# Kernel optimization log

Measured on AMD Instinct MI355X. Metric: run time of the kernel, lower is better.

The kernel has to match this reference:

```python
import jax, jax.numpy as jnp
import numpy as np

N = 30000        # nodes
E = 480000       # edges (before self-loops)
F_IN = 512       # input feature dim
HID = 64         # per-head hidden dim
HEADS = 4
WIDTH = HID * HEADS  # 256, concat heads
LAYERS = 3
NCLS = 40
NEG_SLOPE = 0.2


def setup_inputs() -> dict:
    key = jax.random.key(0)
    ks = jax.random.split(key, 16)
    def p(k, shape, scale=0.1):
        return jax.random.normal(k, shape, dtype=jnp.float32) * scale
    return {
        "x": jax.random.normal(ks[0], (N, F_IN), dtype=jnp.float32),
        "edge_index": jax.random.randint(ks[1], (2, E), 0, N, dtype=jnp.int32),
        # layer 1: F_IN -> HEADS*HID (concat)
        "W1": p(ks[2], (F_IN, WIDTH)), "as1": p(ks[3], (HEADS, HID)), "ad1": p(ks[4], (HEADS, HID)), "b1": p(ks[5], (WIDTH,)),
        # layer 2: WIDTH -> WIDTH
        "W2": p(ks[6], (WIDTH, WIDTH)), "as2": p(ks[7], (HEADS, HID)), "ad2": p(ks[8], (HEADS, HID)), "b2": p(ks[9], (WIDTH,)),
        # layer 3: WIDTH -> WIDTH
        "W3": p(ks[10], (WIDTH, WIDTH)), "as3": p(ks[11], (HEADS, HID)), "ad3": p(ks[12], (HEADS, HID)), "b3": p(ks[13], (WIDTH,)),
        # JK='cat' output head: WIDTH*LAYERS -> NCLS
        "Wo": p(ks[14], (WIDTH * LAYERS, NCLS)), "bo": p(ks[15], (NCLS,)),
    }


def gat_layer(x, Wm, a_src, a_dst, b, src, dst):
    # PyG GATConv (concat=True, eval mode): h = xW reshaped [N,H,C];
    # e_ij = leaky_relu(a_src.h_j + a_dst.h_i) for edge j->i, softmax over dst groups.
    n = x.shape[0]
    H, C = a_src.shape
    h = (x @ Wm).reshape(n, H, C)                      # [N,H,C]
    es = jnp.sum(h * a_src, axis=-1)                   # [N,H]
    ed = jnp.sum(h * a_dst, axis=-1)                   # [N,H]
    e = jax.nn.leaky_relu(es[src] + ed[dst], NEG_SLOPE)  # [Etot,H]
    m = jax.ops.segment_max(e, dst, num_segments=n)    # stable softmax per dst node
    w = jnp.exp(e - m[dst])
    den = jax.ops.segment_sum(w, dst, num_segments=n)
    alpha = w / den[dst]                               # [Etot,H]
    out = jax.ops.segment_sum(h[src] * alpha[:, :, None], dst, num_segments=n)  # [N,H,C]
    return out.reshape(n, H * C) + b


def reference(x, edge_index, W1, as1, ad1, b1, W2, as2, ad2, b2, W3, as3, ad3, b3, Wo, bo):
    # add self-loops (PyG GATConv default)
    loops = jnp.arange(N, dtype=edge_index.dtype)
    src = jnp.concatenate([edge_index[0], loops])
    dst = jnp.concatenate([edge_index[1], loops])
    # dropout is identity in eval mode
    h1 = jax.nn.relu(gat_layer(x, W1, as1, ad1, b1, src, dst))
    h2 = jax.nn.relu(gat_layer(h1, W2, as2, ad2, b2, src, dst))
    h3 = jax.nn.relu(gat_layer(h2, W3, as3, ad3, b3, src, dst))
    h = jnp.concatenate([h1, h2, h3], axis=-1)         # JK 'cat': [N, WIDTH*LAYERS]
    return h @ Wo + bo                                 # [N, NCLS]
```

## Files before the change

### kernel.cpp

```cpp
#include <hip/hip_runtime.h>

#define N_NODES 30000
#define N_EDGES 480000
#define ETOT    510000
#define F_IN    512
#define WIDTH   256
#define NCLS    40
#define KCAT    768
#define NPAD    48

typedef __attribute__((ext_vector_type(8))) short short8;
typedef __attribute__((ext_vector_type(4))) float f32x4;

__device__ __forceinline__ unsigned short f2bf(float f){
  unsigned u = __float_as_uint(f);
  u += 0x7fffu + ((u >> 16) & 1u);
  return (unsigned short)(u >> 16);
}
__device__ __forceinline__ float b2f(unsigned short s){
  return __uint_as_float(((unsigned)s) << 16);
}

__global__ void transpose_w_kernel(const float* __restrict__ W, unsigned short* __restrict__ Wt,
                                   int K, int Nc){
  int k = blockIdx.x * blockDim.x + threadIdx.x;
  int n = blockIdx.y;
  if (k < K) Wt[(size_t)n * K + k] = f2bf(W[(size_t)k * Nc + n]);
}

__global__ void transpose_wo_kernel(const float* __restrict__ Wo, unsigned short* __restrict__ WoT){
  int i = blockIdx.x * blockDim.x + threadIdx.x;
  if (i < NPAD * KCAT){
    int c = i / KCAT, k = i - c * KCAT;
    WoT[i] = (c < NCLS) ? f2bf(Wo[(size_t)k * NCLS + c]) : (unsigned short)0;
  }
}

__global__ void zero_kernel(int* __restrict__ p, int n){
  int i = blockIdx.x * blockDim.x + threadIdx.x;
  if (i < n) p[i] = 0;
}

__global__ void hist_kernel(const int* __restrict__ ei, int* __restrict__ counts){
  int e = blockIdx.x * blockDim.x + threadIdx.x;
  if (e < ETOT){
    int d = (e < N_EDGES) ? ei[N_EDGES + e] : (e - N_EDGES);
    atomicAdd(&counts[d], 1);
  }
}

__global__ __launch_bounds__(1024) void scan_kernel(const int* __restrict__ counts,
                                                    int* __restrict__ offsets,
                                                    int* __restrict__ cursor, int n){
  __shared__ int wsum[16];
  int tid = threadIdx.x, lane = tid & 63, wid = tid >> 6;
  int running = 0;
  int nchunks = (n + 1023) >> 10;
  for (int ch = 0; ch < nchunks; ++ch){
    int i = (ch << 10) + tid;
    int v = (i < n) ? counts[i] : 0;
    int x = v;
    #pragma unroll
    for (int off = 1; off < 64; off <<= 1){
      int t = __shfl_up(x, off, 64);
      if (lane >= off) x += t;
    }
    if (lane == 63) wsum[wid] = x;
    __syncthreads();
    if (wid == 0){
      int s = (lane < 16) ? wsum[lane] : 0;
      #pragma unroll
      for (int off = 1; off < 16; off <<= 1){
        int t = __shfl_up(s, off, 64);
        if (lane >= off) s += t;
      }
      if (lane < 16) wsum[lane] = s;
    }
    __syncthreads();
    int waveprefix = (wid > 0) ? wsum[wid - 1] : 0;
    int excl = x - v + waveprefix + running;
    if (i < n){ offsets[i] = excl; cursor[i] = excl; }
    running += wsum[15];
    __syncthreads();
  }
  if (tid == 0) offsets[n] = running;
}

__global__ void scatter_kernel(const int* __restrict__ ei, int* __restrict__ cursor,
                               int* __restrict__ srcs){
  int e = blockIdx.x * blockDim.x + threadIdx.x;
  if (e < ETOT){
    int s, d;
    if (e < N_EDGES){ s = ei[e]; d = ei[N_EDGES + e]; }
    else { s = e - N_EDGES; d = s; }
    int pos = atomicAdd(&cursor[d], 1);
    srcs[pos] = s;
  }
}

#define BM 64
#define BK 32
#define LDA 40

template<bool AF32>
__global__ __launch_bounds__(256) void gemm_fused_kernel(const void* __restrict__ Araw,
                                                         const unsigned short* __restrict__ Bt,
                                                         const float* __restrict__ a_s,
                                                         const float* __restrict__ a_d,
                                                         float* __restrict__ es,
                                                         float* __restrict__ ed,
                                                         unsigned short* __restrict__ hb,
                                                         int M, int K){
  __shared__ unsigned short Als[BM * LDA];
  __shared__ unsigned short Bls[256 * LDA];
  int tid = threadIdx.x;
  int lane = tid & 63, wid = tid >> 6;
  int l15 = lane & 15, quad = lane >> 4;
  int m0 = blockIdx.x * BM;

  f32x4 acc[16];
  #pragma unroll
  for (int t = 0; t < 16; ++t) acc[t] = (f32x4){0.f, 0.f, 0.f, 0.f};

  for (int k0 = 0; k0 < K; k0 += BK){
    __syncthreads();
    {
      int row = tid >> 2, g = tid & 3;
      int grow = m0 + row; if (grow >= M) grow = M - 1;
      if (AF32){
        const float* Af = (const float*)Araw + (size_t)grow * K + k0 + 8 * g;
        float4 v0 = *(const float4*)(Af);
        float4 v1 = *(const float4*)(Af + 4);
        ushort4 p0 = {f2bf(v0.x), f2bf(v0.y), f2bf(v0.z), f2bf(v0.w)};
        ushort4 p1 = {f2bf(v1.x), f2bf(v1.y), f2bf(v1.z), f2bf(v1.w)};
        *(ushort4*)(&Als[row * LDA + 8 * g])     = p0;
        *(ushort4*)(&Als[row * LDA + 8 * g + 4]) = p1;
      } else {
        const unsigned short* Ab = (const unsigned short*)Araw;
        uint4 av = *(const uint4*)(Ab + (size_t)grow * K + k0 + 8 * g);
        *(uint4*)(&Als[row * LDA + 8 * g]) = av;
      }
      const unsigned short* src = Bt + (size_t)tid * K + k0;
      uint4 b0 = *(const uint4*)(src);
      uint4 b1 = *(const uint4*)(src + 8);
      uint4 b2 = *(const uint4*)(src + 16);
      uint4 b3 = *(const uint4*)(src + 24);
      unsigned short* dst = &Bls[tid * LDA];
      *(uint4*)(dst) = b0;
      *(uint4*)(dst + 8) = b1;
      *(uint4*)(dst + 16) = b2;
      *(uint4*)(dst + 24) = b3;
    }
    __syncthreads();
    short8 af = *(const short8*)(&Als[(16 * wid + l15) * LDA + quad * 8]);
    #pragma unroll
    for (int t = 0; t < 16; ++t){
      short8 bf = *(const short8*)(&Bls[(16 * t + l15) * LDA + quad * 8]);
      acc[t] = __builtin_amdgcn_mfma_f32_16x16x32_bf16(af, bf, acc[t], 0, 0, 0);
    }
  }

  int row0 = m0 + 16 * wid + quad * 4;

  #pragma unroll
  for (int t = 0; t < 16; ++t){
    int col = 16 * t + l15;
    #pragma unroll
    for (int r = 0; r < 4; ++r){
      int grow = row0 + r;
      if (grow < M) hb[(size_t)grow * WIDTH + col] = f2bf(acc[t][r]);
    }
  }

  float as_v[16], ad_v[16];
  #pragma unroll
  for (int t = 0; t < 16; ++t){
    int cc = 16 * (t & 3) + l15;
    as_v[t] = a_s[(t >> 2) * 64 + cc];
    ad_v[t] = a_d[(t >> 2) * 64 + cc];
  }
  #pragma unroll
  for (int h = 0; h < 4; ++h){
    #pragma unroll
    for (int r = 0; r < 4; ++r){
      float se = 0.f, sd = 0.f;
      #pragma unroll
      for (int tt = 0; tt < 4; ++tt){
        int t = 4 * h + tt;
        se += acc[t][r] * as_v[t];
        sd += acc[t][r] * ad_v[t];
      }
      #pragma unroll
      for (int off = 1; off < 16; off <<= 1){
        se += __shfl_xor(se, off, 64);
        sd += __shfl_xor(sd, off, 64);
      }
      int grow = row0 + r;
      if (l15 == 0 && grow < M){
        es[grow * 4 + h] = se;
        ed[grow * 4 + h] = sd;
      }
    }
  }
}

__global__ __launch_bounds__(256) void agg_kernel(const int* __restrict__ offsets,
                                                  const int* __restrict__ srcs,
                                                  const float* __restrict__ es,
                                                  const float* __restrict__ ed,
                                                  const unsigned short* __restrict__ hb,
                                                  const float* __restrict__ bias,
                                                  unsigned short* __restrict__ hout){
  __shared__ float eLds[8][64][4];
  __shared__ int   sLds[8][64];
  int wid = threadIdx.x >> 6;
  int lane = threadIdx.x & 63;
  int half = lane >> 5, l32 = lane & 31;
  int slot = wid * 2 + half;
  int n = blockIdx.x * 8 + slot;
  int base = offsets[n];
  int deg = offsets[n + 1] - base;
  float4 edv = *(const float4*)(ed + n * 4);

  float m0 = -1e30f, m1 = -1e30f, m2 = -1e30f, m3 = -1e30f;
  for (int i = l32; i < deg; i += 32){
    int s = srcs[base + i];
    float4 ev = *(const float4*)(es + s * 4);
    float e0 = ev.x + edv.x, e1 = ev.y + edv.y, e2 = ev.z + edv.z, e3 = ev.w + edv.w;
    e0 = e0 > 0.f ? e0 : 0.2f * e0;
    e1 = e1 > 0.f ? e1 : 0.2f * e1;
    e2 = e2 > 0.f ? e2 : 0.2f * e2;
    e3 = e3 > 0.f ? e3 : 0.2f * e3;
    if (i < 64){
      sLds[slot][i] = s;
      *(float4*)(&eLds[slot][i][0]) = (float4){e0, e1, e2, e3};
    }
    m0 = fmaxf(m0, e0); m1 = fmaxf(m1, e1); m2 = fmaxf(m2, e2); m3 = fmaxf(m3, e3);
  }
  #pragma unroll
  for (int off = 1; off < 32; off <<= 1){
    m0 = fmaxf(m0, __shfl_xor(m0, off, 64));
    m1 = fmaxf(m1, __shfl_xor(m1, off, 64));
    m2 = fmaxf(m2, __shfl_xor(m2, off, 64));
    m3 = fmaxf(m3, __shfl_xor(m3, off, 64));
  }
  int head = l32 >> 3;
  float mh  = (head == 0) ? m0 : (head == 1) ? m1 : (head == 2) ? m2 : m3;
  float edh = (head == 0) ? edv.x : (head == 1) ? edv.y : (head == 2) ? edv.z : edv.w;

  float2 a0 = {0.f,0.f}, a1 = {0.f,0.f}, a2 = {0.f,0.f}, a3 = {0.f,0.f};
  float den = 0.f;
  const unsigned short* hcol = hb + 8 * l32;
  for (int i = 0; i < deg; i += 8){
    int sidx[8]; float w[8];
    #pragma unroll
    for (int u = 0; u < 8; ++u){
      int idx = i + u;
      bool v = idx < deg;
      float le; int s;
      if (idx < 64 || !v){
        int ic = v ? idx : 0;
        if (ic >= 64) ic = 0;
        s  = sLds[slot][ic];
        le = eLds[slot][ic][head];
      } else {
        s = srcs[base + idx];
        float e = es[s * 4 + head] + edh;
        le = e > 0.f ? e : 0.2f * e;
      }
      sidx[u] = s;
      w[u] = v ? __expf(le - mh) : 0.f;
    }
    uint4 hv[8];
    #pragma unroll
    for (int u = 0; u < 8; ++u)
      hv[u] = *(const uint4*)(hcol + (size_t)sidx[u] * WIDTH);
    #pragma unroll
    for (int u = 0; u < 8; ++u){
      float wu = w[u];
      den += wu;
      a0.x += wu * __uint_as_float(hv[u].x << 16);
      a0.y += wu * __uint_as_float(hv[u].x & 0xffff0000u);
      a1.x += wu * __uint_as_float(hv[u].y << 16);
      a1.y += wu * __uint_as_float(hv[u].y & 0xffff0000u);
      a2.x += wu * __uint_as_float(hv[u].z << 16);
      a2.y += wu * __uint_as_float(hv[u].z & 0xffff0000u);
      a3.x += wu * __uint_as_float(hv[u].w << 16);
      a3.y += wu * __uint_as_float(hv[u].w & 0xffff0000u);
    }
  }
  float inv = 1.0f / den;
  const float* bp = bias + 8 * l32;
  float4 bv0 = *(const float4*)(bp);
  float4 bv1 = *(const float4*)(bp + 4);
  float o0 = fmaxf(a0.x * inv + bv0.x, 0.f);
  float o1 = fmaxf(a0.y * inv + bv0.y, 0.f);
  float o2 = fmaxf(a1.x * inv + bv0.z, 0.f);
  float o3 = fmaxf(a1.y * inv + bv0.w, 0.f);
  float o4 = fmaxf(a2.x * inv + bv1.x, 0.f);
  float o5 = fmaxf(a2.y * inv + bv1.y, 0.f);
  float o6 = fmaxf(a3.x * inv + bv1.z, 0.f);
  float o7 = fmaxf(a3.y * inv + bv1.w, 0.f);
  uint4 o;
  o.x = (unsigned)f2bf(o0) | ((unsigned)f2bf(o1) << 16);
  o.y = (unsigned)f2bf(o2) | ((unsigned)f2bf(o3) << 16);
  o.z = (unsigned)f2bf(o4) | ((unsigned)f2bf(o5) << 16);
  o.w = (unsigned)f2bf(o6) | ((unsigned)f2bf(o7) << 16);
  *(uint4*)(hout + (size_t)n * WIDTH + 8 * l32) = o;
}

__global__ __launch_bounds__(256) void out_gemm_kernel(const unsigned short* __restrict__ h1,
                                                       const unsigned short* __restrict__ h2,
                                                       const unsigned short* __restrict__ h3,
                                                       const unsigned short* __restrict__ WoT,
                                                       const float* __restrict__ bo,
                                                       float* __restrict__ out){
  int tid = threadIdx.x, lane = tid & 63, wid = tid >> 6;
  int l15 = lane & 15, quad = lane >> 4;
  int m0 = blockIdx.x * 64 + 16 * wid;

  f32x4 acc[3];
  #pragma unroll
  for (int t = 0; t < 3; ++t) acc[t] = (f32x4){0.f, 0.f, 0.f, 0.f};

  int arow = m0 + l15; if (arow >= N_NODES) arow = N_NODES - 1;

  #pragma unroll
  for (int part = 0; part < 3; ++part){
    const unsigned short* hp = (part == 0) ? h1 : (part == 1) ? h2 : h3;
    const unsigned short* ap = hp + (size_t)arow * WIDTH;
    #pragma unroll
    for (int k0 = 0; k0 < WIDTH; k0 += 32){
      short8 af = *(const short8*)(ap + k0 + quad * 8);
      int kk = part * WIDTH + k0;
      #pragma unroll
      for (int t = 0; t < 3; ++t){
        short8 bf = *(const short8*)(WoT + (size_t)(16 * t + l15) * KCAT + kk + quad * 8);
        acc[t] = __builtin_amdgcn_mfma_f32_16x16x32_bf16(af, bf, acc[t], 0, 0, 0);
      }
    }
  }

  int r0 = m0 + quad * 4;
  #pragma unroll
  for (int t = 0; t < 3; ++t){
    int col = 16 * t + l15;
    if (col < NCLS){
      float bc = bo[col];
      #pragma unroll
      for (int r = 0; r < 4; ++r){
        int grow = r0 + r;
        if (grow < N_NODES) out[(size_t)grow * NCLS + col] = acc[t][r] + bc;
      }
    }
  }
}

static inline size_t align256(size_t x){ return (x + 255) & ~(size_t)255; }

extern "C" void kernel_launch(void* const* d_in, const int* in_sizes, int n_in,
                              void* d_out, int out_size, void* d_ws, size_t ws_size,
                              hipStream_t stream) {
  const float* x   = (const float*)d_in[0];
  const int*   ei  = (const int*)  d_in[1];
  const float* W1  = (const float*)d_in[2];
  const float* as1 = (const float*)d_in[3];
  const float* ad1 = (const float*)d_in[4];
  const float* b1  = (const float*)d_in[5];
  const float* W2  = (const float*)d_in[6];
  const float* as2 = (const float*)d_in[7];
  const float* ad2 = (const float*)d_in[8];
  const float* b2  = (const float*)d_in[9];
  const float* W3  = (const float*)d_in[10];
  const float* as3 = (const float*)d_in[11];
  const float* ad3 = (const float*)d_in[12];
  const float* b3  = (const float*)d_in[13];
  const float* Wo  = (const float*)d_in[14];
  const float* bo  = (const float*)d_in[15];
  float* out = (float*)d_out;

  char* p = (char*)d_ws;
  auto take = [&](size_t bytes) -> char* { char* cur = p; p += align256(bytes); return cur; };

  unsigned short* Wt1   = (unsigned short*)take((size_t)WIDTH * F_IN * 2);
  unsigned short* Wt2   = (unsigned short*)take((size_t)WIDTH * WIDTH * 2);
  unsigned short* Wt3   = (unsigned short*)take((size_t)WIDTH * WIDTH * 2);
  unsigned short* WoT   = (unsigned short*)take((size_t)NPAD * KCAT * 2);
  unsigned short* hstage= (unsigned short*)take((size_t)N_NODES * WIDTH * 2);
  float*          es    = (float*)take((size_t)N_NODES * 4 * 4);
  float*          ed    = (float*)take((size_t)N_NODES * 4 * 4);
  unsigned short* h1b   = (unsigned short*)take((size_t)N_NODES * WIDTH * 2);
  unsigned short* h2b   = (unsigned short*)take((size_t)N_NODES * WIDTH * 2);
  unsigned short* h3b   = (unsigned short*)take((size_t)N_NODES * WIDTH * 2);
  int*            counts  = (int*)take((size_t)N_NODES * 4);
  int*            offsets = (int*)take((size_t)(N_NODES + 1) * 4);
  int*            cursor  = (int*)take((size_t)N_NODES * 4);
  int*            srcs    = (int*)take((size_t)ETOT * 4);

  transpose_w_kernel<<<dim3(F_IN / 256, WIDTH), 256, 0, stream>>>(W1, Wt1, F_IN, WIDTH);
  transpose_w_kernel<<<dim3(1, WIDTH), 256, 0, stream>>>(W2, Wt2, WIDTH, WIDTH);
  transpose_w_kernel<<<dim3(1, WIDTH), 256, 0, stream>>>(W3, Wt3, WIDTH, WIDTH);
  transpose_wo_kernel<<<(NPAD * KCAT + 255) / 256, 256, 0, stream>>>(Wo, WoT);

  zero_kernel<<<(N_NODES + 255) / 256, 256, 0, stream>>>(counts, N_NODES);
  hist_kernel<<<(ETOT + 255) / 256, 256, 0, stream>>>(ei, counts);
  scan_kernel<<<1, 1024, 0, stream>>>(counts, offsets, cursor, N_NODES);
  scatter_kernel<<<(ETOT + 255) / 256, 256, 0, stream>>>(ei, cursor, srcs);

  const int gemm_grid = (N_NODES + BM - 1) / BM;
  const int agg_grid  = N_NODES / 8;

  gemm_fused_kernel<true><<<gemm_grid, 256, 0, stream>>>(x, Wt1, as1, ad1, es, ed, hstage, N_NODES, F_IN);
  agg_kernel<<<agg_grid, 256, 0, stream>>>(offsets, srcs, es, ed, hstage, b1, h1b);
  gemm_fused_kernel<false><<<gemm_grid, 256, 0, stream>>>(h1b, Wt2, as2, ad2, es, ed, hstage, N_NODES, WIDTH);
  agg_kernel<<<agg_grid, 256, 0, stream>>>(offsets, srcs, es, ed, hstage, b2, h2b);
  gemm_fused_kernel<false><<<gemm_grid, 256, 0, stream>>>(h2b, Wt3, as3, ad3, es, ed, hstage, N_NODES, WIDTH);
  agg_kernel<<<agg_grid, 256, 0, stream>>>(offsets, srcs, es, ed, hstage, b3, h3b);

  out_gemm_kernel<<<gemm_grid, 256, 0, stream>>>(h1b, h2b, h3b, WoT, bo, out);
}
```

Measured before the change: 411.6 us.

## Retile GEMM so each wave owns one head's 64 columns with 4x4 MFMA tiles

Each wave now computes all 64 rows for one 64-column head slice (a 4x4 grid of 16x16 MFMA tiles) instead of 16 rows across all 256 columns. Fragments held in registers are reused across tiles, so LDS reads per MFMA go down. The LDS layout moves to k-chunk-major with 8-element groups and no padding. The epilogue packs bf16 pairs through a lane shuffle into 32-bit stores, and each wave computes its head's attention dot products directly. The new LDS layout could introduce bank conflicts, and the shuffle adds work to the epilogue.

```diff
diff --git a/kernel.cpp b/kernel.cpp
--- a/kernel.cpp
+++ b/kernel.cpp
@@ -100,7 +100,6 @@
 
 #define BM 64
 #define BK 32
-#define LDA 40
 
 template<bool AF32>
 __global__ __launch_bounds__(256) void gemm_fused_kernel(const void* __restrict__ Araw,
@@ -111,94 +110,112 @@
                                                          float* __restrict__ ed,
                                                          unsigned short* __restrict__ hb,
                                                          int M, int K){
-  __shared__ unsigned short Als[BM * LDA];
-  __shared__ unsigned short Bls[256 * LDA];
+  __shared__ unsigned short Als[4 * 64 * 8];
+  __shared__ unsigned short Bls[4 * 256 * 8];
   int tid = threadIdx.x;
   int lane = tid & 63, wid = tid >> 6;
   int l15 = lane & 15, quad = lane >> 4;
   int m0 = blockIdx.x * BM;
 
-  f32x4 acc[16];
-  #pragma unroll
-  for (int t = 0; t < 16; ++t) acc[t] = (f32x4){0.f, 0.f, 0.f, 0.f};
+  f32x4 acc[4][4];
+  #pragma unroll
+  for (int rt = 0; rt < 4; ++rt)
+    #pragma unroll
+    for (int ct = 0; ct < 4; ++ct) acc[rt][ct] = (f32x4){0.f, 0.f, 0.f, 0.f};
+
+  int ar = tid & 63, ac = tid >> 6;
+  int agrow = m0 + ar; if (agrow >= M) agrow = M - 1;
 
   for (int k0 = 0; k0 < K; k0 += BK){
     __syncthreads();
+    if (AF32){
+      const float* Af = (const float*)Araw + (size_t)agrow * K + k0 + 8 * ac;
+      float4 v0 = *(const float4*)(Af);
+      float4 v1 = *(const float4*)(Af + 4);
+      ushort4 p0 = {f2bf(v0.x), f2bf(v0.y), f2bf(v0.z), f2bf(v0.w)};
+      ushort4 p1 = {f2bf(v1.x), f2bf(v1.y), f2bf(v1.z), f2bf(v1.w)};
+      *(ushort4*)(&Als[(ac * 64 + ar) * 8])     = p0;
+      *(ushort4*)(&Als[(ac * 64 + ar) * 8 + 4]) = p1;
+    } else {
+      const unsigned short* Ab = (const unsigned short*)Araw;
+      uint4 av = *(const uint4*)(Ab + (size_t)agrow * K + k0 + 8 * ac);
+      *(uint4*)(&Als[(ac * 64 + ar) * 8]) = av;
+    }
     {
-      int row = tid >> 2, g = tid & 3;
-      int grow = m0 + row; if (grow >= M) grow = M - 1;
-      if (AF32){
-        const float* Af = (const float*)Araw + (size_t)grow * K + k0 + 8 * g;
-        float4 v0 = *(const float4*)(Af);
-        float4 v1 = *(const float4*)(Af + 4);
-        ushort4 p0 = {f2bf(v0.x), f2bf(v0.y), f2bf(v0.z), f2bf(v0.w)};
-        ushort4 p1 = {f2bf(v1.x), f2bf(v1.y), f2bf(v1.z), f2bf(v1.w)};
-        *(ushort4*)(&Als[row * LDA + 8 * g])     = p0;
-        *(ushort4*)(&Als[row * LDA + 8 * g + 4]) = p1;
-      } else {
-        const unsigned short* Ab = (const unsigned short*)Araw;
-        uint4 av = *(const uint4*)(Ab + (size_t)grow * K + k0 + 8 * g);
-        *(uint4*)(&Als[row * LDA + 8 * g]) = av;
-      }
       const unsigned short* src = Bt + (size_t)tid * K + k0;
       uint4 b0 = *(const uint4*)(src);
       uint4 b1 = *(const uint4*)(src + 8);
       uint4 b2 = *(const uint4*)(src + 16);
       uint4 b3 = *(const uint4*)(src + 24);
-      unsigned short* dst = &Bls[tid * LDA];
-      *(uint4*)(dst) = b0;
-      *(uint4*)(dst + 8) = b1;
-      *(uint4*)(dst + 16) = b2;
-      *(uint4*)(dst + 24) = b3;
+      *(uint4*)(&Bls[(0 * 256 + tid) * 8]) = b0;
+      *(uint4*)(&Bls[(1 * 256 + tid) * 8]) = b1;
+      *(uint4*)(&Bls[(2 * 256 + tid) * 8]) = b2;
+      *(uint4*)(&Bls[(3 * 256 + tid) * 8]) = b3;
     }
     __syncthreads();
-    short8 af = *(const short8*)(&Als[(16 * wid + l15) * LDA + quad * 8]);
-    #pragma unroll
-    for (int t = 0; t < 16; ++t){
-      short8 bf = *(const short8*)(&Bls[(16 * t + l15) * LDA + quad * 8]);
-      acc[t] = __builtin_amdgcn_mfma_f32_16x16x32_bf16(af, bf, acc[t], 0, 0, 0);
-    }
-  }
-
-  int row0 = m0 + 16 * wid + quad * 4;
-
-  #pragma unroll
-  for (int t = 0; t < 16; ++t){
-    int col = 16 * t + l15;
-    #pragma unroll
-    for (int r = 0; r < 4; ++r){
-      int grow = row0 + r;
-      if (grow < M) hb[(size_t)grow * WIDTH + col] = f2bf(acc[t][r]);
-    }
-  }
-
-  float as_v[16], ad_v[16];
-  #pragma unroll
-  for (int t = 0; t < 16; ++t){
-    int cc = 16 * (t & 3) + l15;
-    as_v[t] = a_s[(t >> 2) * 64 + cc];
-    ad_v[t] = a_d[(t >> 2) * 64 + cc];
-  }
-  #pragma unroll
-  for (int h = 0; h < 4; ++h){
-    #pragma unroll
-    for (int r = 0; r < 4; ++r){
-      float se = 0.f, sd = 0.f;
-      #pragma unroll
-      for (int tt = 0; tt < 4; ++tt){
-        int t = 4 * h + tt;
-        se += acc[t][r] * as_v[t];
-        sd += acc[t][r] * ad_v[t];
-      }
+    short8 af[4], bf[4];
+    #pragma unroll
+    for (int rt = 0; rt < 4; ++rt)
+      af[rt] = *(const short8*)(&Als[(quad * 64 + rt * 16 + l15) * 8]);
+    #pragma unroll
+    for (int ct = 0; ct < 4; ++ct)
+      bf[ct] = *(const short8*)(&Bls[(quad * 256 + wid * 64 + ct * 16 + l15) * 8]);
+    #pragma unroll
+    for (int rt = 0; rt < 4; ++rt)
+      #pragma unroll
+      for (int ct = 0; ct < 4; ++ct)
+        acc[rt][ct] = __builtin_amdgcn_mfma_f32_16x16x32_bf16(af[rt], bf[ct], acc[rt][ct], 0, 0, 0);
+  }
+
+  int colbase = wid * 64;
+
+  #pragma unroll
+  for (int rt = 0; rt < 4; ++rt){
+    int row0 = m0 + rt * 16 + quad * 4;
+    #pragma unroll
+    for (int i = 0; i < 4; ++i){
+      int grow = row0 + i;
+      unsigned vo[4];
+      #pragma unroll
+      for (int ct = 0; ct < 4; ++ct){
+        unsigned lo = (unsigned)f2bf(acc[rt][ct][i]);
+        unsigned hi = (unsigned)__shfl_xor((int)lo, 1, 64);
+        vo[ct] = lo | (hi << 16);
+      }
+      if ((l15 & 1) == 0 && grow < M){
+        unsigned short* hrow = hb + (size_t)grow * WIDTH + colbase + l15;
+        *(unsigned*)(hrow)      = vo[0];
+        *(unsigned*)(hrow + 16) = vo[1];
+        *(unsigned*)(hrow + 32) = vo[2];
+        *(unsigned*)(hrow + 48) = vo[3];
+      }
+    }
+  }
+
+  float asv[4], adv[4];
+  #pragma unroll
+  for (int ct = 0; ct < 4; ++ct){
+    asv[ct] = a_s[wid * 64 + ct * 16 + l15];
+    adv[ct] = a_d[wid * 64 + ct * 16 + l15];
+  }
+  #pragma unroll
+  for (int rt = 0; rt < 4; ++rt){
+    int row0 = m0 + rt * 16 + quad * 4;
+    #pragma unroll
+    for (int i = 0; i < 4; ++i){
+      float se = acc[rt][0][i] * asv[0] + acc[rt][1][i] * asv[1]
+               + acc[rt][2][i] * asv[2] + acc[rt][3][i] * asv[3];
+      float sd = acc[rt][0][i] * adv[0] + acc[rt][1][i] * adv[1]
+               + acc[rt][2][i] * adv[2] + acc[rt][3][i] * adv[3];
       #pragma unroll
       for (int off = 1; off < 16; off <<= 1){
         se += __shfl_xor(se, off, 64);
         sd += __shfl_xor(sd, off, 64);
       }
-      int grow = row0 + r;
+      int grow = row0 + i;
       if (l15 == 0 && grow < M){
-        es[grow * 4 + h] = se;
-        ed[grow * 4 + h] = sd;
+        es[grow * 4 + wid] = se;
+        ed[grow * 4 + wid] = sd;
       }
     }
   }
```

After: 417.2 us. About the same (+1.4%).
